# Kernel tuning notes

Hardware: AMD Instinct MI355X
Metric: run time of the kernel (lower is better)

The kernel has to match this reference:

```python
import jax, jax.numpy as jnp
import numpy as np

B, T, D = 4, 256, 1024
K = 3            # conv kernel size
WIN = 10         # window_size
MARGIN = 2       # margin


def setup_inputs() -> dict:
    key = jax.random.key(0)
    ks = jax.random.split(key, 5)
    features = jax.random.normal(ks[0], (B, T, D), dtype=jnp.float32)
    conv_left_w = jax.random.normal(ks[1], (5, 1, K, K), dtype=jnp.float32) * 0.1
    conv_left_b = jnp.zeros((5,), dtype=jnp.float32)
    conv_right_w = jax.random.normal(ks[2], (5, 1, K, K), dtype=jnp.float32) * 0.1
    conv_right_b = jnp.zeros((5,), dtype=jnp.float32)
    fc_w = jax.random.normal(ks[3], (1, 5), dtype=jnp.float32) * 0.1
    fc_b = jnp.zeros((1,), dtype=jnp.float32)
    return {
        "features": features,
        "conv_left_w": conv_left_w,
        "conv_left_b": conv_left_b,
        "conv_right_w": conv_right_w,
        "conv_right_b": conv_right_b,
        "fc_w": fc_w,
        "fc_b": fc_b,
    }


def _conv2d_same(x, w, b):
    # x: [N, 1, H, W_sp], w: [5, 1, K, K] -> [N, 5, H, W_sp]
    p = (K - 1) // 2
    y = jax.lax.conv_general_dilated(
        x, w, window_strides=(1, 1), padding=((p, p), (p, p)),
        dimension_numbers=("NCHW", "OIHW", "NCHW"))
    return y + b[None, :, None, None]


def reference(features, conv_left_w, conv_left_b, conv_right_w, conv_right_b, fc_w, fc_b):
    b, t, d = features.shape
    w = WIN - MARGIN + 1  # sliding window width (9)
    padded = jnp.pad(features, ((0, 0), (WIN, WIN), (0, 0)))
    left = padded[:, : t + WIN - MARGIN, :]
    right = padded[:, WIN + MARGIN :, :]
    # vectorized unfold: windows start at t' in [0, T), width w
    idx = jnp.arange(t)[:, None] + jnp.arange(w)[None, :]  # [T, w]
    lg = left[:, idx, :]   # [B, T, w, D]
    rg = right[:, idx, :]  # [B, T, w, D]
    # [B*T, 1, D, w]: view(-1,1,w,D) then transpose(-1,-2)
    lg = lg.reshape(b * t, 1, w, d).transpose(0, 1, 3, 2)
    rg = rg.reshape(b * t, 1, w, d).transpose(0, 1, 3, 2)
    x_left = _conv2d_same(lg, conv_left_w, conv_left_b)    # [B*T, 5, D, w]
    x_right = _conv2d_same(rg, conv_right_w, conv_right_b)  # [B*T, 5, D, w]
    x = jnp.concatenate((x_left, x_right), axis=-1)  # [B*T, 5, D, 2w]
    x = x.transpose(0, 2, 3, 1)                      # [B*T, D, 2w, 5]
    x = jnp.einsum("ndwc,oc->ndwo", x, fc_w) + fc_b  # [B*T, D, 2w, 1]
    x = x[..., 0]                                    # [B*T, D, 2w]
    x = jnp.mean(x, axis=-1)                         # adaptive_avg_pool1d -> [B*T, D]
    return x.reshape(b, t, d)
```

## Files before the change

kernel.cpp:

```cpp
#include <hip/hip_runtime.h>

#define BB 4
#define TT 256
#define DD 1024


template <bool SAFE>
__device__ __forceinline__ void compute_taps(
    const float* __restrict__ fb, int t, const float (*wq)[6],
    float4& accA, float4& accB, float4& accE)
{
    float4 v[18];
    #pragma unroll
    for (int i = 0; i < 18; ++i) {
        const int off = (i < 9) ? (i - 10) : (i - 7);
        const int tt = t + off;
        if (SAFE || ((unsigned)tt < TT)) {
            v[i] = *reinterpret_cast<const float4*>(fb + (size_t)tt * DD);
        } else {
            v[i] = make_float4(0.f, 0.f, 0.f, 0.f);
        }
    }

    float4 SL, SR;
    SL.x = ((v[1].x + v[2].x) + (v[3].x + v[4].x)) + ((v[5].x + v[6].x) + v[7].x);
    SL.y = ((v[1].y + v[2].y) + (v[3].y + v[4].y)) + ((v[5].y + v[6].y) + v[7].y);
    SL.z = ((v[1].z + v[2].z) + (v[3].z + v[4].z)) + ((v[5].z + v[6].z) + v[7].z);
    SL.w = ((v[1].w + v[2].w) + (v[3].w + v[4].w)) + ((v[5].w + v[6].w) + v[7].w);
    SR.x = ((v[10].x + v[11].x) + (v[12].x + v[13].x)) + ((v[14].x + v[15].x) + v[16].x);
    SR.y = ((v[10].y + v[11].y) + (v[12].y + v[13].y)) + ((v[14].y + v[15].y) + v[16].y);
    SR.z = ((v[10].z + v[11].z) + (v[12].z + v[13].z)) + ((v[14].z + v[15].z) + v[16].z);
    SR.w = ((v[10].w + v[11].w) + (v[12].w + v[13].w)) + ((v[14].w + v[15].w) + v[16].w);

    float4* accs[3] = { &accA, &accB, &accE };
    #pragma unroll
    for (int kh = 0; kh < 3; ++kh) {
        const float eL0 = wq[kh][0], mL = wq[kh][1], eL8 = wq[kh][2];
        const float eR0 = wq[kh][3], mR = wq[kh][4], eR8 = wq[kh][5];
        float4& a = *accs[kh];
        a.x = eL0*v[0].x + mL*SL.x + eL8*v[8].x + eR0*v[9].x + mR*SR.x + eR8*v[17].x;
        a.y = eL0*v[0].y + mL*SL.y + eL8*v[8].y + eR0*v[9].y + mR*SR.y + eR8*v[17].y;
        a.z = eL0*v[0].z + mL*SL.z + eL8*v[8].z + eR0*v[9].z + mR*SR.z + eR8*v[17].z;
        a.w = eL0*v[0].w + mL*SL.w + eL8*v[8].w + eR0*v[9].w + mR*SR.w + eR8*v[17].w;
    }
}

__global__ __launch_bounds__(256) void sbl_stencil3_kernel(
    const float* __restrict__ feat,
    const float* __restrict__ wl, const float* __restrict__ bl,
    const float* __restrict__ wr, const float* __restrict__ br,
    const float* __restrict__ fcw, const float* __restrict__ fcb,
    float* __restrict__ out)
{
    __shared__ float wq_s[3][6];
    __shared__ float cconst;
    __shared__ float edgeA[4], edgeE[4];

    const int tid = threadIdx.x;
    if (tid < 18) {
        const int kh = tid / 6;
        const int r = tid % 6;
        const int side = r / 3;
        const int which = r % 3;
        const float* W = side ? wr : wl;
        float g0 = 0.f, g1 = 0.f, g2 = 0.f;
        #pragma unroll
        for (int c = 0; c < 5; ++c) {
            const float f = fcw[c];
            g0 += f * W[c * 9 + kh * 3 + 0];
            g1 += f * W[c * 9 + kh * 3 + 1];
            g2 += f * W[c * 9 + kh * 3 + 2];
        }
        const float h = (which == 0) ? (g0 + g1)
                      : (which == 1) ? (g0 + g1 + g2)
                                     : (g1 + g2);
        wq_s[kh][side * 3 + which] = h * (1.0f / 18.0f);
    } else if (tid == 18) {
        float c0 = 0.f;
        #pragma unroll
        for (int c = 0; c < 5; ++c) c0 += fcw[c] * (bl[c] + br[c]);
        cconst = 0.5f * c0 + fcb[0];
    }
    __syncthreads();

    const int blk = blockIdx.x;
    const int b = blk >> 8;
    const int t = blk & 255;
    const int d0 = tid * 4;

    const float* fb = feat + (size_t)b * TT * DD + d0;

    float4 A, Bv, E;
    if (t >= 10 && t <= TT - 11) {
        compute_taps<true>(fb, t, wq_s, A, Bv, E);
    } else {
        compute_taps<false>(fb, t, wq_s, A, Bv, E);
    }

    const int lane = tid & 63;
    const int wv   = tid >> 6;
    float Am1 = __shfl_up(A.w, 1);
    float Ep1 = __shfl_down(E.x, 1);
    if (lane == 63) edgeA[wv] = A.w;
    if (lane == 0)  edgeE[wv] = E.x;
    __syncthreads();
    if (lane == 0)  Am1 = (wv > 0) ? edgeA[wv - 1] : 0.0f;
    if (lane == 63) Ep1 = (wv < 3) ? edgeE[wv + 1] : 0.0f;

    const float C = cconst;
    float4 o;
    o.x = C + Am1 + Bv.x + E.y;
    o.y = C + A.x + Bv.y + E.z;
    o.z = C + A.y + Bv.z + E.w;
    o.w = C + A.z + Bv.w + Ep1;
    *reinterpret_cast<float4*>(out + (size_t)blk * DD + d0) = o;
}

extern "C" void kernel_launch(void* const* d_in, const int* in_sizes, int n_in,
                              void* d_out, int out_size, void* d_ws, size_t ws_size,
                              hipStream_t stream) {
    const float* feat = (const float*)d_in[0];
    const float* wl   = (const float*)d_in[1];
    const float* bl   = (const float*)d_in[2];
    const float* wr   = (const float*)d_in[3];
    const float* br   = (const float*)d_in[4];
    const float* fcw  = (const float*)d_in[5];
    const float* fcb  = (const float*)d_in[6];
    float* out = (float*)d_out;

    dim3 grid(BB * TT);
    dim3 block(256);
    sbl_stencil3_kernel<<<grid, block, 0, stream>>>(feat, wl, bl, wr, br, fcw, fcb, out);
}
```

Measured before the change: 13.00 us.

## Compute four timesteps per block with sliding-window row reuse

Each block now handles four consecutive time rows, loading 24 input rows once instead of 18 rows per output row. Window sums are updated incrementally between rows, and the global loads are issued before the weight-folding prologue so they overlap it. The grid shrinks fourfold to 256 blocks, which lowers parallelism on a large GPU and raises register pressure (launch_bounds 256,1).

Measured after the change: 10.87 us. 16.4% less time.

```diff
diff --git a/kernel.cpp b/kernel.cpp
--- a/kernel.cpp
+++ b/kernel.cpp
@@ -3,49 +3,21 @@
 #define BB 4
 #define TT 256
 #define DD 1024
+#define TC 4
 
-
-template <bool SAFE>
-__device__ __forceinline__ void compute_taps(
-    const float* __restrict__ fb, int t, const float (*wq)[6],
-    float4& accA, float4& accB, float4& accE)
-{
-    float4 v[18];
-    #pragma unroll
-    for (int i = 0; i < 18; ++i) {
-        const int off = (i < 9) ? (i - 10) : (i - 7);
-        const int tt = t + off;
-        if (SAFE || ((unsigned)tt < TT)) {
-            v[i] = *reinterpret_cast<const float4*>(fb + (size_t)tt * DD);
-        } else {
-            v[i] = make_float4(0.f, 0.f, 0.f, 0.f);
-        }
-    }
-
-    float4 SL, SR;
-    SL.x = ((v[1].x + v[2].x) + (v[3].x + v[4].x)) + ((v[5].x + v[6].x) + v[7].x);
-    SL.y = ((v[1].y + v[2].y) + (v[3].y + v[4].y)) + ((v[5].y + v[6].y) + v[7].y);
-    SL.z = ((v[1].z + v[2].z) + (v[3].z + v[4].z)) + ((v[5].z + v[6].z) + v[7].z);
-    SL.w = ((v[1].w + v[2].w) + (v[3].w + v[4].w)) + ((v[5].w + v[6].w) + v[7].w);
-    SR.x = ((v[10].x + v[11].x) + (v[12].x + v[13].x)) + ((v[14].x + v[15].x) + v[16].x);
-    SR.y = ((v[10].y + v[11].y) + (v[12].y + v[13].y)) + ((v[14].y + v[15].y) + v[16].y);
-    SR.z = ((v[10].z + v[11].z) + (v[12].z + v[13].z)) + ((v[14].z + v[15].z) + v[16].z);
-    SR.w = ((v[10].w + v[11].w) + (v[12].w + v[13].w)) + ((v[14].w + v[15].w) + v[16].w);
-
-    float4* accs[3] = { &accA, &accB, &accE };
-    #pragma unroll
-    for (int kh = 0; kh < 3; ++kh) {
-        const float eL0 = wq[kh][0], mL = wq[kh][1], eL8 = wq[kh][2];
-        const float eR0 = wq[kh][3], mR = wq[kh][4], eR8 = wq[kh][5];
-        float4& a = *accs[kh];
-        a.x = eL0*v[0].x + mL*SL.x + eL8*v[8].x + eR0*v[9].x + mR*SR.x + eR8*v[17].x;
-        a.y = eL0*v[0].y + mL*SL.y + eL8*v[8].y + eR0*v[9].y + mR*SR.y + eR8*v[17].y;
-        a.z = eL0*v[0].z + mL*SL.z + eL8*v[8].z + eR0*v[9].z + mR*SR.z + eR8*v[17].z;
-        a.w = eL0*v[0].w + mL*SL.w + eL8*v[8].w + eR0*v[9].w + mR*SR.w + eR8*v[17].w;
-    }
+__device__ __forceinline__ float4 f4zero() { return make_float4(0.f, 0.f, 0.f, 0.f); }
+__device__ __forceinline__ float4 f4add(float4 a, float4 b) {
+    return make_float4(a.x + b.x, a.y + b.y, a.z + b.z, a.w + b.w);
+}
+__device__ __forceinline__ float4 f4sub(float4 a, float4 b) {
+    return make_float4(a.x - b.x, a.y - b.y, a.z - b.z, a.w - b.w);
+}
+__device__ __forceinline__ float4 f4fma(float w, float4 x, float4 acc) {
+    return make_float4(fmaf(w, x.x, acc.x), fmaf(w, x.y, acc.y),
+                       fmaf(w, x.z, acc.z), fmaf(w, x.w, acc.w));
 }
 
-__global__ __launch_bounds__(256) void sbl_stencil3_kernel(
+__global__ __launch_bounds__(256, 1) void sbl_stencil4_kernel(
     const float* __restrict__ feat,
     const float* __restrict__ wl, const float* __restrict__ bl,
     const float* __restrict__ wr, const float* __restrict__ br,
@@ -54,9 +26,30 @@
 {
     __shared__ float wq_s[3][6];
     __shared__ float cconst;
-    __shared__ float edgeA[4], edgeE[4];
+    __shared__ float eA[TC][4], eE[TC][4];
 
     const int tid = threadIdx.x;
+    const int blk = blockIdx.x;
+    const int b  = blk >> 6;
+    const int t0 = (blk & 63) << 2;
+    const int d0 = tid * 4;
+    const float* fb = feat + (size_t)b * TT * DD + d0;
+
+    float4 v[24];
+    if (t0 >= 10 && t0 <= 242) {
+        #pragma unroll
+        for (int i = 0; i < 24; ++i)
+            v[i] = *reinterpret_cast<const float4*>(fb + (size_t)(t0 + i - 10) * DD);
+    } else {
+        #pragma unroll
+        for (int i = 0; i < 24; ++i) {
+            const int row = t0 + i - 10;
+            v[i] = ((unsigned)row < TT)
+                 ? *reinterpret_cast<const float4*>(fb + (size_t)row * DD)
+                 : f4zero();
+        }
+    }
+
     if (tid < 18) {
         const int kh = tid / 6;
         const int r = tid % 6;
@@ -83,37 +76,58 @@
     }
     __syncthreads();
 
-    const int blk = blockIdx.x;
-    const int b = blk >> 8;
-    const int t = blk & 255;
-    const int d0 = tid * 4;
+    float4 SL = f4add(f4add(f4add(v[1], v[2]), f4add(v[3], v[4])),
+                      f4add(f4add(v[5], v[6]), v[7]));
+    float4 SR = f4add(f4add(f4add(v[13], v[14]), f4add(v[15], v[16])),
+                      f4add(f4add(v[17], v[18]), v[19]));
 
-    const float* fb = feat + (size_t)b * TT * DD + d0;
-
-    float4 A, Bv, E;
-    if (t >= 10 && t <= TT - 11) {
-        compute_taps<true>(fb, t, wq_s, A, Bv, E);
-    } else {
-        compute_taps<false>(fb, t, wq_s, A, Bv, E);
+    float4 A[TC], Bv[TC], E[TC];
+    #pragma unroll
+    for (int j = 0; j < TC; ++j) {
+        if (j > 0) {
+            SL = f4add(f4sub(SL, v[j]), v[j + 7]);
+            SR = f4add(f4sub(SR, v[j + 12]), v[j + 19]);
+        }
+        #pragma unroll
+        for (int kh = 0; kh < 3; ++kh) {
+            float4 a = f4zero();
+            a = f4fma(wq_s[kh][0], v[j],      a);
+            a = f4fma(wq_s[kh][1], SL,        a);
+            a = f4fma(wq_s[kh][2], v[j + 8],  a);
+            a = f4fma(wq_s[kh][3], v[j + 12], a);
+            a = f4fma(wq_s[kh][4], SR,        a);
+            a = f4fma(wq_s[kh][5], v[j + 20], a);
+            if (kh == 0) A[j] = a; else if (kh == 1) Bv[j] = a; else E[j] = a;
+        }
     }
 
     const int lane = tid & 63;
     const int wv   = tid >> 6;
-    float Am1 = __shfl_up(A.w, 1);
-    float Ep1 = __shfl_down(E.x, 1);
-    if (lane == 63) edgeA[wv] = A.w;
-    if (lane == 0)  edgeE[wv] = E.x;
+    if (lane == 63) {
+        #pragma unroll
+        for (int j = 0; j < TC; ++j) eA[j][wv] = A[j].w;
+    }
+    if (lane == 0) {
+        #pragma unroll
+        for (int j = 0; j < TC; ++j) eE[j][wv] = E[j].x;
+    }
     __syncthreads();
-    if (lane == 0)  Am1 = (wv > 0) ? edgeA[wv - 1] : 0.0f;
-    if (lane == 63) Ep1 = (wv < 3) ? edgeE[wv + 1] : 0.0f;
 
     const float C = cconst;
-    float4 o;
-    o.x = C + Am1 + Bv.x + E.y;
-    o.y = C + A.x + Bv.y + E.z;
-    o.z = C + A.y + Bv.z + E.w;
-    o.w = C + A.z + Bv.w + Ep1;
-    *reinterpret_cast<float4*>(out + (size_t)blk * DD + d0) = o;
+    float* ob = out + ((size_t)(b * TT + t0) * DD + d0);
+    #pragma unroll
+    for (int j = 0; j < TC; ++j) {
+        float Am1 = __shfl_up(A[j].w, 1);
+        float Ep1 = __shfl_down(E[j].x, 1);
+        if (lane == 0)  Am1 = (wv > 0) ? eA[j][wv - 1] : 0.0f;
+        if (lane == 63) Ep1 = (wv < 3) ? eE[j][wv + 1] : 0.0f;
+        float4 o;
+        o.x = C + Am1    + Bv[j].x + E[j].y;
+        o.y = C + A[j].x + Bv[j].y + E[j].z;
+        o.z = C + A[j].y + Bv[j].z + E[j].w;
+        o.w = C + A[j].z + Bv[j].w + Ep1;
+        *reinterpret_cast<float4*>(ob + (size_t)j * DD) = o;
+    }
 }
 
 extern "C" void kernel_launch(void* const* d_in, const int* in_sizes, int n_in,
@@ -128,7 +142,7 @@
     const float* fcb  = (const float*)d_in[6];
     float* out = (float*)d_out;
 
-    dim3 grid(BB * TT);
+    dim3 grid(BB * (TT / TC));
     dim3 block(256);
-    sbl_stencil3_kernel<<<grid, block, 0, stream>>>(feat, wl, bl, wr, br, fcw, fcb, out);
+    sbl_stencil4_kernel<<<grid, block, 0, stream>>>(feat, wl, bl, wr, br, fcw, fcb, out);
 }
```
